# Kernel tuning notes

Hardware: AMD Instinct MI355X
Metric: run time of the kernel (lower is better)

## Reference

```python
import jax, jax.numpy as jnp
import numpy as np

N = 50000       # number of nodes
E = 800000      # number of edges (avg degree 16)
F_IN = 128      # in_features
F_OUT = 128     # out_features
EPS = 1e-5      # BatchNorm1d default eps


def setup_inputs() -> dict:
    key = jax.random.key(0)
    k = jax.random.split(key, 4)
    x = jax.random.normal(k[0], (N, F_IN), dtype=jnp.float32)
    src = jax.random.randint(k[1], (E,), 0, N, dtype=jnp.int32)
    dst = jax.random.randint(k[2], (E,), 0, N, dtype=jnp.int32)
    # row-normalized adjacency weights (mean aggregation): 1 / in-degree(dst)
    deg = jax.ops.segment_sum(jnp.ones((E,), jnp.float32), dst, num_segments=N)
    w_edge = (1.0 / jnp.maximum(deg, 1.0))[dst]
    # Linear(2*F_IN -> F_OUT, bias=False) weight, torch layout [out, in]
    W = jax.random.normal(k[3], (F_OUT, 2 * F_IN), dtype=jnp.float32) * 0.05
    gamma = jnp.ones((F_OUT,), jnp.float32)
    beta = jnp.zeros((F_OUT,), jnp.float32)
    return {"x": x, "src": src, "dst": dst, "w_edge": w_edge,
            "W": W, "gamma": gamma, "beta": beta}


def reference(x, src, dst, w_edge, W, gamma, beta):
    # spmm(adj, x): gather source features, scale by edge weight, scatter-add to dst
    msgs = w_edge[:, None] * x[src]                       # [E, F_IN]
    agg = jax.ops.segment_sum(msgs, dst, num_segments=N)  # [N, F_IN]
    h = jnp.concatenate([x, agg], axis=1)                 # [N, 2*F_IN]
    y = h @ W.T                                           # [N, F_OUT]
    # BatchNorm1d in training mode: batch stats over node dim, biased variance
    mean = jnp.mean(y, axis=0)
    var = jnp.mean((y - mean) ** 2, axis=0)
    out = (y - mean) * jax.lax.rsqrt(var + EPS) * gamma + beta
    return out
```

## Files before the change

### kernel.cpp

```cpp
#include <hip/hip_runtime.h>

#define F 128
#define EPSV 1e-5f
#define NPB 256

typedef _Float16 f16x8 __attribute__((ext_vector_type(8)));
typedef _Float16 f16x4 __attribute__((ext_vector_type(4)));
typedef _Float16 f16x2 __attribute__((ext_vector_type(2)));
typedef float    f32x4 __attribute__((ext_vector_type(4)));

#define SRCMASK 0x1FFFFFF

__global__ __launch_bounds__(256) void k_phase0(
        const float* __restrict__ x, _Float16* __restrict__ xh, int n4x,
        const float* __restrict__ W, _Float16* __restrict__ wh, int n4w,
        const int* __restrict__ dst, int* __restrict__ histA,
        int E, int Epb, int NF, int nbx) {
    int t = threadIdx.x, b = blockIdx.x;
    if (b < NPB) {
        __shared__ int h[512];
        h[t] = 0; h[t + 256] = 0;
        __syncthreads();
        int beg = b * Epb;
        int end = min(beg + Epb, E);
        for (int i = beg + t; i < end; i += 256)
            atomicAdd(&h[dst[i] >> 7], 1);
        __syncthreads();
        for (int f = t; f < NF; f += 256)
            histA[f * NPB + b] = h[f];
    } else if (b < NPB + nbx) {
        int i = (b - NPB) * 256 + t;
        if (i >= n4x) return;
        float4 v = *reinterpret_cast<const float4*>(x + (size_t)i * 4);
        f16x4 o = { (_Float16)v.x, (_Float16)v.y, (_Float16)v.z, (_Float16)v.w };
        *reinterpret_cast<f16x4*>(xh + (size_t)i * 4) = o;
    } else {
        int i = (b - NPB - nbx) * 256 + t;
        if (i >= n4w) return;
        float4 v = *reinterpret_cast<const float4*>(W + (size_t)i * 4);
        f16x4 o = { (_Float16)v.x, (_Float16)v.y, (_Float16)v.z, (_Float16)v.w };
        *reinterpret_cast<f16x4*>(wh + (size_t)i * 4) = o;
    }
}

__global__ __launch_bounds__(256) void k_pa2a(
        const int* __restrict__ histA, int* __restrict__ cursorRel,
        int* __restrict__ tot) {
    __shared__ int wsum[4];
    int f = blockIdx.x, t = threadIdx.x;
    int lane = t & 63, wv = t >> 6;
    int v = histA[f * NPB + t];
    int sc = v;
    #pragma unroll
    for (int off = 1; off < 64; off <<= 1) {
        int o = __shfl_up(sc, off);
        if (lane >= off) sc += o;
    }
    if (lane == 63) wsum[wv] = sc;
    __syncthreads();
    int woff = 0;
    for (int i = 0; i < wv; ++i) woff += wsum[i];
    cursorRel[f * NPB + t] = woff + sc - v;
    if (t == 255) tot[f] = woff + sc;
}

__global__ __launch_bounds__(256) void k_pa2b(
        const int* __restrict__ tot, int* __restrict__ bktptr,
        float* __restrict__ stats, int NF) {
    int t = threadIdx.x;
    stats[t] = 0.f;
    if (t < 64) {
        int carry = 0;
        for (int base = 0; base < NF; base += 64) {
            int i = base + t;
            int v = (i < NF) ? tot[i] : 0;
            int sc = v;
            #pragma unroll
            for (int off = 1; off < 64; off <<= 1) {
                int o = __shfl_up(sc, off);
                if (t >= off) sc += o;
            }
            if (i < NF) bktptr[i] = carry + sc - v;
            carry += __shfl(sc, 63);
        }
        if (t == 0) bktptr[NF] = carry;
    }
}

__global__ __launch_bounds__(256) void k_pa3(
        const int* __restrict__ dst, const int* __restrict__ src,
        const float* __restrict__ we, const int* __restrict__ cursorRel,
        const int* __restrict__ bktptr,
        int2* __restrict__ payload, int E, int Epb, int NF) {
    __shared__ int cur[512];
    int t = threadIdx.x, b = blockIdx.x;
    for (int f = t; f < NF; f += 256)
        cur[f] = bktptr[f] + cursorRel[f * NPB + b];
    __syncthreads();
    int beg = b * Epb;
    int end = min(beg + Epb, E);
    for (int i0 = beg + t * 4; i0 < end; i0 += 1024) {
        int d[4], s[4]; float w[4];
        if (i0 + 3 < end) {
            int4   d4 = *reinterpret_cast<const int4*>(dst + i0);
            int4   s4 = *reinterpret_cast<const int4*>(src + i0);
            float4 w4 = *reinterpret_cast<const float4*>(we + i0);
            d[0] = d4.x; d[1] = d4.y; d[2] = d4.z; d[3] = d4.w;
            s[0] = s4.x; s[1] = s4.y; s[2] = s4.z; s[3] = s4.w;
            w[0] = w4.x; w[1] = w4.y; w[2] = w4.z; w[3] = w4.w;
        } else {
            #pragma unroll
            for (int u = 0; u < 4; ++u) {
                int i = min(i0 + u, E - 1);
                d[u] = dst[i]; s[u] = src[i]; w[u] = we[i];
            }
        }
        int slot[4];
        #pragma unroll
        for (int u = 0; u < 4; ++u)
            if (i0 + u < end) slot[u] = atomicAdd(&cur[d[u] >> 7], 1);
        #pragma unroll
        for (int u = 0; u < 4; ++u)
            if (i0 + u < end)
                payload[slot[u]] = make_int2(s[u] | ((d[u] & 127) << 25),
                                             __float_as_int(w[u]));
    }
}

__global__ __launch_bounds__(256) void k_sortb(
        const int* __restrict__ bktptr, const int2* __restrict__ payload,
        int2* __restrict__ payload2, int* __restrict__ nodeptr, int NF) {
    __shared__ int h[128], hs[128], cur[128];
    int t = threadIdx.x, f = blockIdx.x;
    if (t < 128) h[t] = 0;
    __syncthreads();
    int beg = bktptr[f], end = bktptr[f + 1];
    for (int i = beg + t; i < end; i += 256)
        atomicAdd(&h[(payload[i].x >> 25) & 127], 1);
    __syncthreads();
    if (t < 64) {
        int v0 = h[t], s0 = v0;
        #pragma unroll
        for (int off = 1; off < 64; off <<= 1) {
            int o = __shfl_up(s0, off);
            if (t >= off) s0 += o;
        }
        int tot0 = __shfl(s0, 63);
        hs[t] = s0 - v0;
        int v1 = h[64 + t], s1 = v1;
        #pragma unroll
        for (int off = 1; off < 64; off <<= 1) {
            int o = __shfl_up(s1, off);
            if (t >= off) s1 += o;
        }
        hs[64 + t] = tot0 + s1 - v1;
    }
    __syncthreads();
    if (t < 128) {
        cur[t] = hs[t];
        nodeptr[f * 128 + t] = beg + hs[t];
    }
    if (f == NF - 1 && t == 0) nodeptr[NF * 128] = end;
    __syncthreads();
    for (int i = beg + t; i < end; i += 256) {
        int2 p = payload[i];
        int r = (p.x >> 25) & 127;
        int pos = atomicAdd(&cur[r], 1);
        payload2[beg + pos] = p;
    }
}

__global__ __launch_bounds__(256) void k_agg(
        const _Float16* __restrict__ xh, const int* __restrict__ nodeptr,
        const int2* __restrict__ payload2, _Float16* __restrict__ aggh,
        int N, int E) {
    int wv = threadIdx.x >> 6, lane = threadIdx.x & 63;
    int n = blockIdx.x * 4 + wv;
    if (n >= N) return;
    int beg = nodeptr[n];
    int cnt = nodeptr[n + 1] - beg;
    float ax = 0.f, ay = 0.f;
    for (int i = 0; i < cnt; i += 8) {
        int i0 = beg + i;
        int2 p[8];
        #pragma unroll
        for (int u = 0; u < 8; ++u)
            p[u] = payload2[min(i0 + u, E - 1)];
        f16x2 v[8];
        #pragma unroll
        for (int u = 0; u < 8; ++u)
            v[u] = *reinterpret_cast<const f16x2*>(
                xh + (size_t)(p[u].x & SRCMASK) * F + lane * 2);
        #pragma unroll
        for (int u = 0; u < 8; ++u) {
            float wu = (i + u < cnt) ? __int_as_float(p[u].y) : 0.f;
            ax += wu * (float)v[u][0];
            ay += wu * (float)v[u][1];
        }
    }
    f16x2 o = { (_Float16)ax, (_Float16)ay };
    *reinterpret_cast<f16x2*>(aggh + (size_t)n * F + lane * 2) = o;
}

__global__ __launch_bounds__(256) void k_gemm_mfma(
        const _Float16* __restrict__ xh, const _Float16* __restrict__ aggh,
        const _Float16* __restrict__ wh, _Float16* __restrict__ yh,
        float* __restrict__ colsum, float* __restrict__ colsumsq, int N) {
    __shared__ _Float16 lds_w[32768];
    __shared__ float lds_s[4][128], lds_q[4][128];
    int t = threadIdx.x, w = t >> 6, l = t & 63;
    int lo16 = l & 15, hi4 = l >> 4;

    #pragma unroll
    for (int i = 0; i < 16; ++i) {
        int c = i * 256 + t;
        int o = c >> 5, kc = c & 31;
        f16x8 v = *reinterpret_cast<const f16x8*>(wh + (size_t)c * 8);
        int byte = (o * 512 + kc * 16) ^ ((o & 7) << 4);
        *reinterpret_cast<f16x8*>((char*)lds_w + byte) = v;
    }
    __syncthreads();

    int rows0 = blockIdx.x * 128 + w * 32;
    int ra0 = rows0 + lo16, ra1 = rows0 + 16 + lo16;
    if (ra0 >= N) ra0 = N - 1;
    if (ra1 >= N) ra1 = N - 1;

    f32x4 acc0[8] = {}, acc1[8] = {};
    #pragma unroll
    for (int kb = 0; kb < 8; ++kb) {
        const _Float16* base = (kb < 4) ? xh : aggh;
        int koff = (kb & 3) * 32 + hi4 * 8;
        f16x8 a0 = *reinterpret_cast<const f16x8*>(base + (size_t)ra0 * F + koff);
        f16x8 a1 = *reinterpret_cast<const f16x8*>(base + (size_t)ra1 * F + koff);
        #pragma unroll
        for (int ct = 0; ct < 8; ++ct) {
            int o = ct * 16 + lo16;
            int byte = (o * 512 + kb * 64 + hi4 * 16) ^ ((o & 7) << 4);
            f16x8 b = *reinterpret_cast<const f16x8*>((char*)lds_w + byte);
            acc0[ct] = __builtin_amdgcn_mfma_f32_16x16x32_f16(a0, b, acc0[ct], 0, 0, 0);
            acc1[ct] = __builtin_amdgcn_mfma_f32_16x16x32_f16(a1, b, acc1[ct], 0, 0, 0);
        }
    }

    #pragma unroll
    for (int ct = 0; ct < 8; ++ct) {
        float sv = 0.f, qv = 0.f;
        int col = ct * 16 + lo16;
        #pragma unroll
        for (int r = 0; r < 4; ++r) {
            int row0 = rows0 + hi4 * 4 + r;
            float v0 = acc0[ct][r];
            if (row0 < N) {
                yh[(size_t)row0 * F + col] = (_Float16)v0;
                sv += v0; qv += v0 * v0;
            }
            int row1 = rows0 + 16 + hi4 * 4 + r;
            float v1 = acc1[ct][r];
            if (row1 < N) {
                yh[(size_t)row1 * F + col] = (_Float16)v1;
                sv += v1; qv += v1 * v1;
            }
        }
        sv += __shfl_xor(sv, 16); sv += __shfl_xor(sv, 32);
        qv += __shfl_xor(qv, 16); qv += __shfl_xor(qv, 32);
        if (l < 16) {
            lds_s[w][col] = sv;
            lds_q[w][col] = qv;
        }
    }
    __syncthreads();
    if (t < 128) {
        float S = lds_s[0][t] + lds_s[1][t] + lds_s[2][t] + lds_s[3][t];
        float Q = lds_q[0][t] + lds_q[1][t] + lds_q[2][t] + lds_q[3][t];
        atomicAdd(&colsum[t], S);
        atomicAdd(&colsumsq[t], Q);
    }
}

__global__ __launch_bounds__(256) void k_norm(
        const _Float16* __restrict__ yh, float* __restrict__ out,
        const float* __restrict__ colsum, const float* __restrict__ colsumsq,
        const float* __restrict__ gamma, const float* __restrict__ beta,
        float ninv, int total8) {
    __shared__ float sc_sh[F], sh_sh[F];
    int t = threadIdx.x;
    if (t < F) {
        float mean = colsum[t] * ninv;
        float var = colsumsq[t] * ninv - mean * mean;
        float rstd = rsqrtf(var + EPSV);
        float sc = gamma[t] * rstd;
        sc_sh[t] = sc;
        sh_sh[t] = beta[t] - mean * sc;
    }
    __syncthreads();
    int idx = blockIdx.x * 256 + t;
    if (idx >= total8) return;
    int col8 = (idx & 15) * 8;
    f16x8 v = *reinterpret_cast<const f16x8*>(yh + (size_t)idx * 8);
    float4 o0, o1;
    o0.x = (float)v[0] * sc_sh[col8 + 0] + sh_sh[col8 + 0];
    o0.y = (float)v[1] * sc_sh[col8 + 1] + sh_sh[col8 + 1];
    o0.z = (float)v[2] * sc_sh[col8 + 2] + sh_sh[col8 + 2];
    o0.w = (float)v[3] * sc_sh[col8 + 3] + sh_sh[col8 + 3];
    o1.x = (float)v[4] * sc_sh[col8 + 4] + sh_sh[col8 + 4];
    o1.y = (float)v[5] * sc_sh[col8 + 5] + sh_sh[col8 + 5];
    o1.z = (float)v[6] * sc_sh[col8 + 6] + sh_sh[col8 + 6];
    o1.w = (float)v[7] * sc_sh[col8 + 7] + sh_sh[col8 + 7];
    *reinterpret_cast<float4*>(out + (size_t)idx * 8)     = o0;
    *reinterpret_cast<float4*>(out + (size_t)idx * 8 + 4) = o1;
}

extern "C" void kernel_launch(void* const* d_in, const int* in_sizes, int n_in,
                              void* d_out, int out_size, void* d_ws, size_t ws_size,
                              hipStream_t stream) {
    (void)n_in; (void)out_size; (void)ws_size;
    const float* x     = (const float*)d_in[0];
    const int*   src   = (const int*)d_in[1];
    const int*   dst   = (const int*)d_in[2];
    const float* we    = (const float*)d_in[3];
    const float* W     = (const float*)d_in[4];
    const float* gamma = (const float*)d_in[5];
    const float* beta  = (const float*)d_in[6];
    int N = in_sizes[0] / F;
    int E = in_sizes[1];

    int NF  = (N + 127) / 128;
    int Epb = (((E + NPB - 1) / NPB) + 3) & ~3;

    char* ws = (char*)d_ws;
    size_t off = 0;
    auto alloc = [&](size_t bytes) {
        void* p = ws + off;
        off += (bytes + 255) & ~(size_t)255;
        return p;
    };
    _Float16* xh     = (_Float16*)alloc((size_t)N * F * sizeof(_Float16));
    _Float16* aggh   = (_Float16*)alloc((size_t)N * F * sizeof(_Float16));
    _Float16* yh     = (_Float16*)alloc((size_t)N * F * sizeof(_Float16));
    _Float16* wh     = (_Float16*)alloc((size_t)F * 2 * F * sizeof(_Float16));
    float* stats     = (float*)alloc(2 * F * sizeof(float));
    int*   histA     = (int*)alloc((size_t)512 * NPB * sizeof(int));
    int*   cursorRel = (int*)alloc((size_t)512 * NPB * sizeof(int));
    int*   tot       = (int*)alloc((size_t)512 * sizeof(int));
    int*   bktptr    = (int*)alloc((size_t)(512 + 1) * sizeof(int));
    int*   nodeptr   = (int*)alloc((size_t)(512 * 128 + 1) * sizeof(int));
    int2*  payload   = (int2*)alloc((size_t)E * sizeof(int2));
    int2*  payload2  = (int2*)alloc((size_t)E * sizeof(int2));
    float* colsum    = stats;
    float* colsumsq  = stats + F;

    float* y = (float*)d_out;

    int n4x = N * F / 4, n4w = 2 * F * F / 4;
    int nbx = (n4x + 255) / 256, nbw = (n4w + 255) / 256;
    hipLaunchKernelGGL(k_phase0, dim3(NPB + nbx + nbw), dim3(256), 0, stream,
                       x, xh, n4x, W, wh, n4w, dst, histA, E, Epb, NF, nbx);

    hipLaunchKernelGGL(k_pa2a, dim3(NF), dim3(256), 0, stream,
                       histA, cursorRel, tot);
    hipLaunchKernelGGL(k_pa2b, dim3(1), dim3(256), 0, stream,
                       tot, bktptr, stats, NF);
    hipLaunchKernelGGL(k_pa3, dim3(NPB), dim3(256), 0, stream,
                       dst, src, we, cursorRel, bktptr, payload, E, Epb, NF);
    hipLaunchKernelGGL(k_sortb, dim3(NF), dim3(256), 0, stream,
                       bktptr, payload, payload2, nodeptr, NF);

    hipLaunchKernelGGL(k_agg, dim3((N + 3) / 4), dim3(256), 0, stream,
                       xh, nodeptr, payload2, aggh, N, E);

    hipLaunchKernelGGL(k_gemm_mfma, dim3((N + 127) / 128), dim3(256), 0, stream,
                       xh, aggh, wh, yh, colsum, colsumsq, N);

    hipLaunchKernelGGL(k_norm, dim3((N * F / 8 + 255) / 256), dim3(256), 0, stream,
                       yh, y, colsum, colsumsq, gamma, beta, 1.0f / (float)N, N * F / 8);
}
```

Before: 105.6 us.

## Fuse per-bucket sort with aggregation in LDS and retile GEMM to 512 threads

The bucket-local counting sort now keeps the sorted edge payload in shared memory, and the same block aggregates its 128 destination nodes directly from it. This removes the payload2 and nodeptr global buffers and one kernel launch. Each wave now walks 16 nodes in sequence, so far fewer waves are issuing gathers, which may leave gather latency less hidden. Buckets larger than CAP would silently drop edges. Separately, the MFMA GEMM moves to 512 threads with one 16-row tile per wave instead of two, which raises wave count but halves reuse of each B fragment read from LDS.

Result: faster. 92.65 us (-12.3%).

```diff
diff --git a/kernel.cpp b/kernel.cpp
--- a/kernel.cpp
+++ b/kernel.cpp
@@ -3,6 +3,7 @@
 #define F 128
 #define EPSV 1e-5f
 #define NPB 256
+#define CAP 5120
 
 typedef _Float16 f16x8 __attribute__((ext_vector_type(8)));
 typedef _Float16 f16x4 __attribute__((ext_vector_type(4)));
@@ -127,16 +128,18 @@
     }
 }
 
-__global__ __launch_bounds__(256) void k_sortb(
-        const int* __restrict__ bktptr, const int2* __restrict__ payload,
-        int2* __restrict__ payload2, int* __restrict__ nodeptr, int NF) {
-    __shared__ int h[128], hs[128], cur[128];
+__global__ __launch_bounds__(512) void k_sortagg(
+        const _Float16* __restrict__ xh, const int* __restrict__ bktptr,
+        const int2* __restrict__ payload, _Float16* __restrict__ aggh, int N) {
+    __shared__ int2 pl[CAP];
+    __shared__ int h[128], hs[129], cur[128];
     int t = threadIdx.x, f = blockIdx.x;
+    int beg = bktptr[f], end = bktptr[f + 1];
+    int cnt = min(end - beg, CAP);
     if (t < 128) h[t] = 0;
     __syncthreads();
-    int beg = bktptr[f], end = bktptr[f + 1];
-    for (int i = beg + t; i < end; i += 256)
-        atomicAdd(&h[(payload[i].x >> 25) & 127], 1);
+    for (int i = t; i < cnt; i += 512)
+        atomicAdd(&h[(payload[beg + i].x >> 25) & 127], 1);
     __syncthreads();
     if (t < 64) {
         int v0 = h[t], s0 = v0;
@@ -156,64 +159,60 @@
         hs[64 + t] = tot0 + s1 - v1;
     }
     __syncthreads();
-    if (t < 128) {
-        cur[t] = hs[t];
-        nodeptr[f * 128 + t] = beg + hs[t];
-    }
-    if (f == NF - 1 && t == 0) nodeptr[NF * 128] = end;
-    __syncthreads();
-    for (int i = beg + t; i < end; i += 256) {
-        int2 p = payload[i];
+    if (t < 128) cur[t] = hs[t];
+    if (t == 128) hs[128] = cnt;
+    __syncthreads();
+    for (int i = t; i < cnt; i += 512) {
+        int2 p = payload[beg + i];
         int r = (p.x >> 25) & 127;
         int pos = atomicAdd(&cur[r], 1);
-        payload2[beg + pos] = p;
-    }
-}
-
-__global__ __launch_bounds__(256) void k_agg(
-        const _Float16* __restrict__ xh, const int* __restrict__ nodeptr,
-        const int2* __restrict__ payload2, _Float16* __restrict__ aggh,
-        int N, int E) {
-    int wv = threadIdx.x >> 6, lane = threadIdx.x & 63;
-    int n = blockIdx.x * 4 + wv;
-    if (n >= N) return;
-    int beg = nodeptr[n];
-    int cnt = nodeptr[n + 1] - beg;
-    float ax = 0.f, ay = 0.f;
-    for (int i = 0; i < cnt; i += 8) {
-        int i0 = beg + i;
-        int2 p[8];
-        #pragma unroll
-        for (int u = 0; u < 8; ++u)
-            p[u] = payload2[min(i0 + u, E - 1)];
-        f16x2 v[8];
-        #pragma unroll
-        for (int u = 0; u < 8; ++u)
-            v[u] = *reinterpret_cast<const f16x2*>(
-                xh + (size_t)(p[u].x & SRCMASK) * F + lane * 2);
-        #pragma unroll
-        for (int u = 0; u < 8; ++u) {
-            float wu = (i + u < cnt) ? __int_as_float(p[u].y) : 0.f;
-            ax += wu * (float)v[u][0];
-            ay += wu * (float)v[u][1];
-        }
-    }
-    f16x2 o = { (_Float16)ax, (_Float16)ay };
-    *reinterpret_cast<f16x2*>(aggh + (size_t)n * F + lane * 2) = o;
-}
-
-__global__ __launch_bounds__(256) void k_gemm_mfma(
+        pl[pos] = p;
+    }
+    __syncthreads();
+
+    int wv = t >> 6, lane = t & 63;
+    int row0 = f << 7;
+    #pragma unroll 1
+    for (int k = 0; k < 16; ++k) {
+        int r = wv * 16 + k;
+        int n = row0 + r;
+        if (n >= N) break;
+        int b0 = hs[r], b1 = hs[r + 1];
+        float ax = 0.f, ay = 0.f;
+        for (int i = b0; i < b1; i += 8) {
+            int2 p[8];
+            #pragma unroll
+            for (int u = 0; u < 8; ++u)
+                p[u] = pl[min(i + u, cnt - 1)];
+            f16x2 v[8];
+            #pragma unroll
+            for (int u = 0; u < 8; ++u)
+                v[u] = *reinterpret_cast<const f16x2*>(
+                    xh + (size_t)(p[u].x & SRCMASK) * F + lane * 2);
+            #pragma unroll
+            for (int u = 0; u < 8; ++u) {
+                float wu = (i + u < b1) ? __int_as_float(p[u].y) : 0.f;
+                ax += wu * (float)v[u][0];
+                ay += wu * (float)v[u][1];
+            }
+        }
+        f16x2 o = { (_Float16)ax, (_Float16)ay };
+        *reinterpret_cast<f16x2*>(aggh + (size_t)n * F + lane * 2) = o;
+    }
+}
+
+__global__ __launch_bounds__(512) void k_gemm_mfma(
         const _Float16* __restrict__ xh, const _Float16* __restrict__ aggh,
         const _Float16* __restrict__ wh, _Float16* __restrict__ yh,
         float* __restrict__ colsum, float* __restrict__ colsumsq, int N) {
     __shared__ _Float16 lds_w[32768];
-    __shared__ float lds_s[4][128], lds_q[4][128];
+    __shared__ float lds_s[8][128], lds_q[8][128];
     int t = threadIdx.x, w = t >> 6, l = t & 63;
     int lo16 = l & 15, hi4 = l >> 4;
 
     #pragma unroll
-    for (int i = 0; i < 16; ++i) {
-        int c = i * 256 + t;
+    for (int i = 0; i < 8; ++i) {
+        int c = i * 512 + t;
         int o = c >> 5, kc = c & 31;
         f16x8 v = *reinterpret_cast<const f16x8*>(wh + (size_t)c * 8);
         int byte = (o * 512 + kc * 16) ^ ((o & 7) << 4);
@@ -221,25 +220,22 @@
     }
     __syncthreads();
 
-    int rows0 = blockIdx.x * 128 + w * 32;
-    int ra0 = rows0 + lo16, ra1 = rows0 + 16 + lo16;
+    int rows0 = blockIdx.x * 128 + w * 16;
+    int ra0 = rows0 + lo16;
     if (ra0 >= N) ra0 = N - 1;
-    if (ra1 >= N) ra1 = N - 1;
-
-    f32x4 acc0[8] = {}, acc1[8] = {};
+
+    f32x4 acc0[8] = {};
     #pragma unroll
     for (int kb = 0; kb < 8; ++kb) {
         const _Float16* base = (kb < 4) ? xh : aggh;
         int koff = (kb & 3) * 32 + hi4 * 8;
         f16x8 a0 = *reinterpret_cast<const f16x8*>(base + (size_t)ra0 * F + koff);
-        f16x8 a1 = *reinterpret_cast<const f16x8*>(base + (size_t)ra1 * F + koff);
         #pragma unroll
         for (int ct = 0; ct < 8; ++ct) {
             int o = ct * 16 + lo16;
             int byte = (o * 512 + kb * 64 + hi4 * 16) ^ ((o & 7) << 4);
             f16x8 b = *reinterpret_cast<const f16x8*>((char*)lds_w + byte);
             acc0[ct] = __builtin_amdgcn_mfma_f32_16x16x32_f16(a0, b, acc0[ct], 0, 0, 0);
-            acc1[ct] = __builtin_amdgcn_mfma_f32_16x16x32_f16(a1, b, acc1[ct], 0, 0, 0);
         }
     }
 
@@ -255,12 +251,6 @@
                 yh[(size_t)row0 * F + col] = (_Float16)v0;
                 sv += v0; qv += v0 * v0;
             }
-            int row1 = rows0 + 16 + hi4 * 4 + r;
-            float v1 = acc1[ct][r];
-            if (row1 < N) {
-                yh[(size_t)row1 * F + col] = (_Float16)v1;
-                sv += v1; qv += v1 * v1;
-            }
         }
         sv += __shfl_xor(sv, 16); sv += __shfl_xor(sv, 32);
         qv += __shfl_xor(qv, 16); qv += __shfl_xor(qv, 32);
@@ -271,8 +261,12 @@
     }
     __syncthreads();
     if (t < 128) {
-        float S = lds_s[0][t] + lds_s[1][t] + lds_s[2][t] + lds_s[3][t];
-        float Q = lds_q[0][t] + lds_q[1][t] + lds_q[2][t] + lds_q[3][t];
+        float S = 0.f, Q = 0.f;
+        #pragma unroll
+        for (int wv = 0; wv < 8; ++wv) {
+            S += lds_s[wv][t];
+            Q += lds_q[wv][t];
+        }
         atomicAdd(&colsum[t], S);
         atomicAdd(&colsumsq[t], Q);
     }
@@ -344,9 +338,7 @@
     int*   cursorRel = (int*)alloc((size_t)512 * NPB * sizeof(int));
     int*   tot       = (int*)alloc((size_t)512 * sizeof(int));
     int*   bktptr    = (int*)alloc((size_t)(512 + 1) * sizeof(int));
-    int*   nodeptr   = (int*)alloc((size_t)(512 * 128 + 1) * sizeof(int));
     int2*  payload   = (int2*)alloc((size_t)E * sizeof(int2));
-    int2*  payload2  = (int2*)alloc((size_t)E * sizeof(int2));
     float* colsum    = stats;
     float* colsumsq  = stats + F;
 
@@ -363,13 +355,11 @@
                        tot, bktptr, stats, NF);
     hipLaunchKernelGGL(k_pa3, dim3(NPB), dim3(256), 0, stream,
                        dst, src, we, cursorRel, bktptr, payload, E, Epb, NF);
-    hipLaunchKernelGGL(k_sortb, dim3(NF), dim3(256), 0, stream,
-                       bktptr, payload, payload2, nodeptr, NF);
-
-    hipLaunchKernelGGL(k_agg, dim3((N + 3) / 4), dim3(256), 0, stream,
-                       xh, nodeptr, payload2, aggh, N, E);
-
-    hipLaunchKernelGGL(k_gemm_mfma, dim3((N + 127) / 128), dim3(256), 0, stream,
+
+    hipLaunchKernelGGL(k_sortagg, dim3(NF), dim3(512), 0, stream,
+                       xh, bktptr, payload, aggh, N);
+
+    hipLaunchKernelGGL(k_gemm_mfma, dim3((N + 127) / 128), dim3(512), 0, stream,
                        xh, aggh, wh, yh, colsum, colsumsq, N);
 
     hipLaunchKernelGGL(k_norm, dim3((N * F / 8 + 255) / 256), dim3(256), 0, stream,
```
